# Performance work log

Hardware: AMD Instinct MI355X
Metric: run time of the kernel (lower is better)

The kernel has to match this reference:

```python
import jax, jax.numpy as jnp
import numpy as np

ZP = -1e10  # zero_padding log-prob fill from the original module


def _transition(prev, same_tr):
    # prev: (B, P) log-probs over path states; CTC allowed transitions: stay, +1, +2 (skip blank)
    s1 = jnp.pad(prev[:, :-1], ((0, 0), (1, 0)), constant_values=ZP)
    s2 = jnp.pad(prev[:, :-2], ((0, 0), (2, 0)), constant_values=ZP)
    # +2 transition forbidden when path[t] == path[t-2] (same label separated by blank)
    s2 = s2.at[:, 2:].set(jnp.where(same_tr, ZP, s2[:, 2:]))
    return jax.nn.logsumexp(jnp.stack([prev, s1, s2], axis=0), axis=0)


def _ctc_loss(x, targets):
    # x: (N, C, S) unnormalized logits; original does log(softmax) == log_softmax
    logy = jax.nn.log_softmax(jnp.transpose(x, (2, 0, 1)), axis=2)  # (T, B, C)
    T, B, _ = logy.shape
    L = targets.shape[1]
    P = 2 * L + 1
    # blank(=0)-interleaved path: [blank, l1, blank, l2, ..., blank]
    path = jnp.zeros((B, P), jnp.int32).at[:, 1::2].set(targets.astype(jnp.int32))
    # emission log-probs gathered at path states: (T, B, P)
    emit = jnp.take_along_axis(logy, jnp.broadcast_to(path[None], (T, B, P)), axis=2)
    same = path[:, 2:] == path[:, :-2]  # (B, P-2)
    init = jnp.full((B, P), ZP, jnp.float32).at[:, 0].set(0.0)

    # forward pass: alpha_t = transition(alpha_{t-1}) + emission_t
    def fstep(alpha, e_t):
        a = _transition(alpha, same) + e_t
        return a, a

    _, alphas = jax.lax.scan(fstep, init, emit)  # (T, B, P)

    # backward pass on time-and-label flipped lattice (input/path lengths are uniform
    # in the original module, so flipping == pure reversal)
    same_r = same[:, ::-1]
    emit_r = emit[::-1, :, ::-1]
    alphas_f = alphas[::-1, :, ::-1]

    def bstep(beta, inp):
        a_f, e_r = inp
        new = _transition(beta, same_r)  # beta transition without current emission
        return new + e_r, a_f + new  # combined = alpha + beta'

    _, comb_f = jax.lax.scan(bstep, init, (alphas_f, emit_r))
    combined = comb_f[::-1, :, ::-1]  # (T, B, P)
    # total log-likelihood read off at t=0
    return -jax.nn.logsumexp(combined[0], axis=1)  # (B,)


def setup_inputs():
    key = jax.random.key(0)
    k1, k2 = jax.random.split(key)
    x = jax.random.normal(k1, (64, 256, 2048), dtype=jnp.float32)
    # labels in [1, 255]; 0 is the blank symbol
    targets = jax.random.randint(k2, (64, 128), 0, 255, dtype=jnp.int32) + 1
    return {"x": x, "targets": targets}


def reference(x, targets):
    return _ctc_loss(x, targets)
```

## Files before the change

kernel.cpp:

```cpp
#include <hip/hip_runtime.h>

#define ZP (-1.0e10f)

constexpr int TT = 2048;
constexpr int BB = 64;
constexpr int CC = 256;
constexpr int LL = 128;
constexpr int PP = 2 * LL + 1;
constexpr int HT = TT / 2;
constexpr int SPL = 5;
constexpr int PADP = 260;
constexpr int NDEN = 512;

__device__ __forceinline__ float lse3f(float a, float b, float c) {
  float m = fmaxf(fmaxf(a, b), c);
  float s = __expf(a - m) + __expf(b - m) + __expf(c - m);
  return m + __logf(s);
}
__device__ __forceinline__ float lse2f(float a, float b) {
  float m = fmaxf(a, b);
  return m + __logf(__expf(a - m) + __expf(b - m));
}

__device__ __forceinline__ int path_at(const int* __restrict__ tg, int p) {
  return (p & 1) ? tg[p >> 1] : 0;
}

__global__ __launch_bounds__(256) void ctc_main(
    const float* __restrict__ x, const int* __restrict__ tgt,
    float* __restrict__ S, float* __restrict__ wsA, float* __restrict__ wsB) {
  const int bid = blockIdx.x;

  if (bid < 2 * BB) {
    if (threadIdx.x >= 64) return;
    const int lane = threadIdx.x;
    const int b = bid & (BB - 1);
    const bool bwd = (bid >= BB);
    const int* tg = tgt + b * LL;
    const float* xb = x + (size_t)b * CC * TT;
    const int pbase = lane * SPL;

    bool valid[SPL];
    bool alw[SPL];
    const float* rp[SPL];
    float af[SPL];
    #pragma unroll
    for (int j = 0; j < SPL; ++j) {
      const int p = pbase + j;
      const bool v = (p < PP);
      valid[j] = v;
      int row = 0;
      if (v && (p & 1)) row = tg[p >> 1];
      rp[j] = xb + (size_t)row * TT;
      if (!bwd) {
        af[j] = (p == 0) ? 0.0f : ZP;
        alw[j] = (v && p >= 2) ? (path_at(tg, p) != path_at(tg, p - 2)) : false;
      } else {
        af[j] = (p == PP - 1) ? 0.0f : ZP;
        alw[j] = (v && (p + 2 < PP)) ? (path_at(tg, p) != path_at(tg, p + 2)) : false;
      }
    }

    if (!bwd) {
      float4 cur[SPL], nxt[SPL];
      #pragma unroll
      for (int j = 0; j < SPL; ++j) cur[j] = *(const float4*)(rp[j]);
      for (int tb = 0; tb < HT; tb += 4) {
        #pragma unroll
        for (int j = 0; j < SPL; ++j) nxt[j] = *(const float4*)(rp[j] + tb + 4);
        #pragma unroll
        for (int k = 0; k < 4; ++k) {
          float up4 = __shfl_up(af[4], 1);
          float up3 = __shfl_up(af[3], 1);
          if (lane == 0) { up4 = ZP; up3 = ZP; }
          const float pm1[SPL] = {up4, af[0], af[1], af[2], af[3]};
          const float pm2[SPL] = {up3, up4, af[0], af[1], af[2]};
          float na[SPL];
          #pragma unroll
          for (int j = 0; j < SPL; ++j) {
            const float em = (k == 0) ? cur[j].x : (k == 1) ? cur[j].y
                           : (k == 2) ? cur[j].z : cur[j].w;
            na[j] = lse3f(af[j], pm1[j], alw[j] ? pm2[j] : ZP) + em;
          }
          #pragma unroll
          for (int j = 0; j < SPL; ++j) af[j] = valid[j] ? na[j] : ZP;
        }
        #pragma unroll
        for (int j = 0; j < SPL; ++j) cur[j] = nxt[j];
      }
      #pragma unroll
      for (int j = 0; j < SPL; ++j)
        if (valid[j]) wsA[b * PADP + pbase + j] = af[j];
    } else {
      float4 cur[SPL], nxt[SPL];
      #pragma unroll
      for (int j = 0; j < SPL; ++j) cur[j] = *(const float4*)(rp[j] + TT - 4);
      for (int tb = TT - 4; tb >= HT; tb -= 4) {
        const int tn = (tb - 4 >= 0) ? tb - 4 : 0;
        #pragma unroll
        for (int j = 0; j < SPL; ++j) nxt[j] = *(const float4*)(rp[j] + tn);
        #pragma unroll
        for (int k = 3; k >= 0; --k) {
          float dn0 = __shfl_down(af[0], 1);
          float dn1 = __shfl_down(af[1], 1);
          const float pp1[SPL] = {af[1], af[2], af[3], af[4], dn0};
          const float pp2[SPL] = {af[2], af[3], af[4], dn0, dn1};
          float na[SPL];
          #pragma unroll
          for (int j = 0; j < SPL; ++j) {
            const float em = (k == 0) ? cur[j].x : (k == 1) ? cur[j].y
                           : (k == 2) ? cur[j].z : cur[j].w;
            na[j] = lse3f(af[j], pp1[j], alw[j] ? pp2[j] : ZP) + em;
          }
          #pragma unroll
          for (int j = 0; j < SPL; ++j) af[j] = valid[j] ? na[j] : ZP;
        }
        #pragma unroll
        for (int j = 0; j < SPL; ++j) cur[j] = nxt[j];
      }
      #pragma unroll
      for (int j = 0; j < SPL; ++j)
        if (valid[j]) wsB[b * PADP + pbase + j] = af[j];
    }
    return;
  }

  const int d = bid - 2 * BB;
  const int b = d >> 3;
  const int t = ((d & 7) << 8) + threadIdx.x;
  const float* xp = x + (size_t)b * CC * TT + t;
  float m = -1e30f, s = 0.0f;
  #pragma unroll 4
  for (int c = 0; c < CC; ++c) {
    const float v = xp[(size_t)c * TT];
    const float nm = fmaxf(m, v);
    s = s * __expf(m - nm) + __expf(v - nm);
    m = nm;
  }
  float dl = m + __logf(s);
  #pragma unroll
  for (int off = 1; off < 64; off <<= 1) dl += __shfl_xor(dl, off);
  if ((threadIdx.x & 63) == 0) atomicAdd(&S[b], dl);
}

__global__ __launch_bounds__(64) void ctc_final(
    const int* __restrict__ tgt, const float* __restrict__ S,
    const float* __restrict__ wsA, const float* __restrict__ wsB,
    float* __restrict__ out) {
  const int b = blockIdx.x;
  const int lane = threadIdx.x;
  const int* tg = tgt + b * LL;
  const int pbase = lane * SPL;

  float a[SPL], bt[SPL];
  bool valid[SPL], alw[SPL];
  #pragma unroll
  for (int j = 0; j < SPL; ++j) {
    const int p = pbase + j;
    const bool v = (p < PP);
    valid[j] = v;
    a[j] = v ? wsA[b * PADP + p] : ZP;
    bt[j] = v ? wsB[b * PADP + p] : ZP;
    alw[j] = (v && (p + 2 < PP)) ? (path_at(tg, p) != path_at(tg, p + 2)) : false;
  }
  const float dn0 = __shfl_down(bt[0], 1);
  const float dn1 = __shfl_down(bt[1], 1);
  const float pp1[SPL] = {bt[1], bt[2], bt[3], bt[4], dn0};
  const float pp2[SPL] = {bt[2], bt[3], bt[4], dn0, dn1};
  float v = ZP;
  #pragma unroll
  for (int j = 0; j < SPL; ++j) {
    if (valid[j]) {
      const float comb = a[j] + lse3f(bt[j], pp1[j], alw[j] ? pp2[j] : ZP);
      v = lse2f(v, comb);
    }
  }
  #pragma unroll
  for (int off = 1; off < 64; off <<= 1) v = lse2f(v, __shfl_xor(v, off));
  if (lane == 0) out[b] = S[b] - v;
}

extern "C" void kernel_launch(void* const* d_in, const int* in_sizes, int n_in,
                              void* d_out, int out_size, void* d_ws, size_t ws_size,
                              hipStream_t stream) {
  const float* x = (const float*)d_in[0];
  const int* tgt = (const int*)d_in[1];
  float* out = (float*)d_out;

  float* S = (float*)d_ws;
  float* wsA = S + 64;
  float* wsB = wsA + BB * PADP;

  hipMemsetAsync(d_ws, 0, 64 * sizeof(float), stream);
  ctc_main<<<dim3(2 * BB + NDEN), dim3(256), 0, stream>>>(x, tgt, S, wsA, wsB);
  ctc_final<<<dim3(BB), dim3(64), 0, stream>>>(tgt, S, wsA, wsB, out);
}
```

Baseline: 489.4 us.

## Pre-gather emissions into bf16 path-ordered buffer before recursion

Adds a prep kernel that gathers the path-state emission rows of x into a contiguous workspace buffer. The buffer is stored in bf16, pre-scaled by log2(e) and rotated per row to spread memory channels. The recursion kernel then reads this compact buffer and works in base-2 (exp2/log2), so the serial forward/backward loop does half-width loads from a smaller, prefetch-friendly region instead of strided fp32 rows. It adds an extra pass over the gathered data and a workspace requirement, with a fallback to the old kernel if the workspace is too small. bf16 emissions also reduce numerical precision.

```diff
diff --git a/kernel.cpp b/kernel.cpp
--- a/kernel.cpp
+++ b/kernel.cpp
@@ -11,6 +11,8 @@
 constexpr int SPL = 5;
 constexpr int PADP = 260;
 constexpr int NDEN = 512;
+constexpr int NROWG = PADP / 4;
+constexpr int NGATH = BB * NROWG;
 
 __device__ __forceinline__ float lse3f(float a, float b, float c) {
   float m = fmaxf(fmaxf(a, b), c);
@@ -21,16 +23,159 @@
   float m = fmaxf(a, b);
   return m + __logf(__expf(a - m) + __expf(b - m));
 }
-
+__device__ __forceinline__ float lse3_2(float a, float b, float c) {
+  float m = fmaxf(fmaxf(a, b), c);
+  return m + __log2f(exp2f(a - m) + exp2f(b - m) + exp2f(c - m));
+}
 __device__ __forceinline__ int path_at(const int* __restrict__ tg, int p) {
   return (p & 1) ? tg[p >> 1] : 0;
 }
-
-__global__ __launch_bounds__(256) void ctc_main(
+__device__ __forceinline__ float bf2f(unsigned short u) {
+  return __uint_as_float(((unsigned)u) << 16);
+}
+__device__ __forceinline__ unsigned short f2bf(float f) {
+  unsigned u = __float_as_uint(f);
+  unsigned r = (u + 0x7fffu + ((u >> 16) & 1u)) >> 16;
+  return (unsigned short)r;
+}
+
+__global__ __launch_bounds__(256) void ctc_prep(
+    const float* __restrict__ x, const int* __restrict__ tgt,
+    float* __restrict__ S, unsigned short* __restrict__ E) {
+  const int bid = blockIdx.x;
+  if (bid < NGATH) {
+    const int b = bid / NROWG;
+    const int p = (bid % NROWG) * 4 + (threadIdx.x >> 6);
+    const int lane = threadIdx.x & 63;
+    unsigned short* __restrict__ Er = E + ((size_t)(b * PADP + p)) * TT;
+    if (p >= PP) {
+      const unsigned short PB = f2bf(-1.0e9f);
+      ushort4 z = {PB, PB, PB, PB};
+      #pragma unroll
+      for (int j = 0; j < 8; ++j) ((ushort4*)Er)[lane + j * 64] = z;
+      return;
+    }
+    const int row = (p & 1) ? tgt[b * LL + (p >> 1)] : 0;
+    const float4* __restrict__ xr = (const float4*)(x + ((size_t)b * CC + row) * TT);
+    const int rot4 = (p * 17) & 511;
+    const float L2E = 1.4426950408889634f;
+    #pragma unroll
+    for (int j = 0; j < 8; ++j) {
+      const int t4 = lane + j * 64;
+      float4 v = xr[t4];
+      ushort4 o;
+      o.x = f2bf(v.x * L2E); o.y = f2bf(v.y * L2E);
+      o.z = f2bf(v.z * L2E); o.w = f2bf(v.w * L2E);
+      ((ushort4*)Er)[(t4 + rot4) & 511] = o;
+    }
+    return;
+  }
+  const int d = bid - NGATH;
+  const int b = d >> 3;
+  const int t = ((d & 7) << 8) + threadIdx.x;
+  const float* xp = x + (size_t)b * CC * TT + t;
+  float m = -1e30f, s = 0.0f;
+  #pragma unroll 4
+  for (int c = 0; c < CC; ++c) {
+    const float v = xp[(size_t)c * TT];
+    const float nm = fmaxf(m, v);
+    s = s * __expf(m - nm) + __expf(v - nm);
+    m = nm;
+  }
+  float dl = m + __logf(s);
+  #pragma unroll
+  for (int off = 1; off < 64; off <<= 1) dl += __shfl_xor(dl, off);
+  if ((threadIdx.x & 63) == 0) atomicAdd(&S[b], dl);
+}
+
+#define LDV(dst, t4v) { _Pragma("unroll") \
+  for (int j = 0; j < SPL; ++j) \
+    dst[j] = *(const ushort4*)(Er[j] + ((((t4v) + rot4[j]) & 511) << 2)); }
+
+#define FSTEPL(B, C) { \
+  float u4 = __shfl_up(af[4], 1); \
+  float u3 = __shfl_up(af[3], 1); \
+  if (lane == 0) { u4 = ZP; u3 = ZP; } \
+  float n0 = lse3_2(af[0], u4,    alw[0] ? u3    : ZP) + bf2f(B[0].C); \
+  float n1 = lse3_2(af[1], af[0], alw[1] ? u4    : ZP) + bf2f(B[1].C); \
+  float n2 = lse3_2(af[2], af[1], alw[2] ? af[0] : ZP) + bf2f(B[2].C); \
+  float n3 = lse3_2(af[3], af[2], alw[3] ? af[1] : ZP) + bf2f(B[3].C); \
+  float n4 = lse3_2(af[4], af[3], alw[4] ? af[2] : ZP) + bf2f(B[4].C); \
+  af[0] = n0; af[1] = n1; af[2] = n2; af[3] = n3; af[4] = n4; }
+
+#define BSTEPL(B, C) { \
+  float d0 = __shfl_down(af[0], 1); \
+  float d1 = __shfl_down(af[1], 1); \
+  float n4 = lse3_2(af[4], d0,    alw[4] ? d1    : ZP) + bf2f(B[4].C); \
+  float n3 = lse3_2(af[3], af[4], alw[3] ? d0    : ZP) + bf2f(B[3].C); \
+  float n2 = lse3_2(af[2], af[3], alw[2] ? af[4] : ZP) + bf2f(B[2].C); \
+  float n1 = lse3_2(af[1], af[2], alw[1] ? af[3] : ZP) + bf2f(B[1].C); \
+  float n0 = lse3_2(af[0], af[1], alw[0] ? af[2] : ZP) + bf2f(B[0].C); \
+  af[0] = n0; af[1] = n1; af[2] = n2; af[3] = n3; af[4] = n4; }
+
+__global__ __launch_bounds__(64) void ctc_rec(
+    const unsigned short* __restrict__ E, const int* __restrict__ tgt,
+    float* __restrict__ wsA, float* __restrict__ wsB) {
+  const int lane = threadIdx.x;
+  const int b = blockIdx.x & (BB - 1);
+  const bool bwd = blockIdx.x >= BB;
+  const int* tg = tgt + b * LL;
+  const int pbase = lane * SPL;
+  const float LN2 = 0.6931471805599453f;
+
+  const unsigned short* Er[SPL];
+  int rot4[SPL];
+  bool alw[SPL];
+  float af[SPL];
+  #pragma unroll
+  for (int j = 0; j < SPL; ++j) {
+    const int p = pbase + j;
+    const int pc = (p < PADP) ? p : (PADP - 1);
+    Er[j] = E + ((size_t)(b * PADP + pc)) * TT;
+    rot4[j] = (pc * 17) & 511;
+    if (!bwd) alw[j] = (p < PP) && (p >= 2) && (path_at(tg, p) != path_at(tg, p - 2));
+    else      alw[j] = (p < PP) && (p + 2 < PP) && (path_at(tg, p) != path_at(tg, p + 2));
+    af[j] = ZP;
+    if (!bwd && p == 0) af[j] = 0.0f;
+    if (bwd && p == PP - 1) af[j] = 0.0f;
+  }
+  ushort4 cur[SPL], nxt[SPL];
+
+  if (!bwd) {
+    LDV(cur, 0);
+    for (int t4 = 0; t4 < 256; ++t4) {
+      const int tn = (t4 + 1 < 256) ? t4 + 1 : 255;
+      LDV(nxt, tn);
+      FSTEPL(cur, x) FSTEPL(cur, y) FSTEPL(cur, z) FSTEPL(cur, w)
+      #pragma unroll
+      for (int j = 0; j < SPL; ++j) cur[j] = nxt[j];
+    }
+    #pragma unroll
+    for (int j = 0; j < SPL; ++j) {
+      const int p = pbase + j;
+      if (p < PP) wsA[b * PADP + p] = af[j] * LN2;
+    }
+  } else {
+    LDV(cur, 511);
+    for (int t4 = 511; t4 >= 256; --t4) {
+      const int tn = (t4 - 1 >= 256) ? t4 - 1 : 256;
+      LDV(nxt, tn);
+      BSTEPL(cur, w) BSTEPL(cur, z) BSTEPL(cur, y) BSTEPL(cur, x)
+      #pragma unroll
+      for (int j = 0; j < SPL; ++j) cur[j] = nxt[j];
+    }
+    #pragma unroll
+    for (int j = 0; j < SPL; ++j) {
+      const int p = pbase + j;
+      if (p < PP) wsB[b * PADP + p] = af[j] * LN2;
+    }
+  }
+}
+
+__global__ __launch_bounds__(256) void ctc_main_fb(
     const float* __restrict__ x, const int* __restrict__ tgt,
     float* __restrict__ S, float* __restrict__ wsA, float* __restrict__ wsB) {
   const int bid = blockIdx.x;
-
   if (bid < 2 * BB) {
     if (threadIdx.x >= 64) return;
     const int lane = threadIdx.x;
@@ -39,11 +184,7 @@
     const int* tg = tgt + b * LL;
     const float* xb = x + (size_t)b * CC * TT;
     const int pbase = lane * SPL;
-
-    bool valid[SPL];
-    bool alw[SPL];
-    const float* rp[SPL];
-    float af[SPL];
+    bool valid[SPL]; bool alw[SPL]; const float* rp[SPL]; float af[SPL];
     #pragma unroll
     for (int j = 0; j < SPL; ++j) {
       const int p = pbase + j;
@@ -60,7 +201,6 @@
         alw[j] = (v && (p + 2 < PP)) ? (path_at(tg, p) != path_at(tg, p + 2)) : false;
       }
     }
-
     if (!bwd) {
       float4 cur[SPL], nxt[SPL];
       #pragma unroll
@@ -124,7 +264,6 @@
     }
     return;
   }
-
   const int d = bid - 2 * BB;
   const int b = d >> 3;
   const int t = ((d & 7) << 8) + threadIdx.x;
@@ -151,7 +290,6 @@
   const int lane = threadIdx.x;
   const int* tg = tgt + b * LL;
   const int pbase = lane * SPL;
-
   float a[SPL], bt[SPL];
   bool valid[SPL], alw[SPL];
   #pragma unroll
@@ -190,8 +328,15 @@
   float* S = (float*)d_ws;
   float* wsA = S + 64;
   float* wsB = wsA + BB * PADP;
+  unsigned short* E = (unsigned short*)(wsB + BB * PADP);
+  const size_t need = (size_t)(64 + 2 * BB * PADP) * 4 + (size_t)BB * PADP * TT * 2;
 
   hipMemsetAsync(d_ws, 0, 64 * sizeof(float), stream);
-  ctc_main<<<dim3(2 * BB + NDEN), dim3(256), 0, stream>>>(x, tgt, S, wsA, wsB);
+  if (ws_size >= need) {
+    ctc_prep<<<dim3(NGATH + NDEN), dim3(256), 0, stream>>>(x, tgt, S, E);
+    ctc_rec<<<dim3(2 * BB), dim3(64), 0, stream>>>(E, tgt, wsA, wsB);
+  } else {
+    ctc_main_fb<<<dim3(2 * BB + NDEN), dim3(256), 0, stream>>>(x, tgt, S, wsA, wsB);
+  }
   ctc_final<<<dim3(BB), dim3(64), 0, stream>>>(tgt, S, wsA, wsB, out);
 }
```

Result: slower. 603.1 us (+23.2%).
